# Kernel optimization log

Hardware: AMD Instinct MI355X
Metric: run time of the kernel (lower is better)

Reference implementation:

```python
import jax, jax.numpy as jnp
import numpy as np

N = 50000
E = 800000
H = 128

def _mlp_init(key, sizes, bias_flags):
    ws = []
    for i, (din, dout) in enumerate(zip(sizes[:-1], sizes[1:])):
        key, k1, k2 = jax.random.split(key, 3)
        lim = 1.0 / np.sqrt(din)
        W = jax.random.uniform(k1, (din, dout), jnp.float32, -lim, lim)
        ws.append(W)
        if bias_flags[i]:
            ws.append(jax.random.uniform(k2, (dout,), jnp.float32, -lim, lim))
    return key, ws

def setup_inputs() -> dict:
    key = jax.random.key(0)
    key, kh, kx, ke = jax.random.split(key, 4)
    h = jax.random.normal(kh, (N, H), jnp.float32)
    x = jax.random.normal(kx, (N, 3), jnp.float32)
    edge_index = jax.random.randint(ke, (2, E), 0, N, jnp.int64)
    # edge_mlp: Linear(2H+1, H), Linear(H, H), both with bias
    key, (W_e1, b_e1, W_e2, b_e2) = _mlp_init(key, [2 * H + 1, H, H], [True, True])
    # coord_mlp: Linear(H, H) with bias, Linear(H, 1) no bias
    key, (W_c1, b_c1, W_c2) = _mlp_init(key, [H, H, 1], [True, False])
    # node_mlp: Linear(2H, H), Linear(H, H), both with bias
    key, (W_n1, b_n1, W_n2, b_n2) = _mlp_init(key, [2 * H, H, H], [True, True])
    ln_g = jnp.ones((H,), jnp.float32)
    ln_b = jnp.zeros((H,), jnp.float32)
    return {"h": h, "x": x, "edge_index": edge_index,
            "W_e1": W_e1, "b_e1": b_e1, "W_e2": W_e2, "b_e2": b_e2,
            "W_c1": W_c1, "b_c1": b_c1, "W_c2": W_c2,
            "W_n1": W_n1, "b_n1": b_n1, "W_n2": W_n2, "b_n2": b_n2,
            "ln_g": ln_g, "ln_b": ln_b}

def reference(h, x, edge_index, W_e1, b_e1, W_e2, b_e2, W_c1, b_c1, W_c2,
              W_n1, b_n1, W_n2, b_n2, ln_g, ln_b):
    row, col = edge_index[0], edge_index[1]
    coord_diff = x[row] - x[col]                       # [E, 3]
    dist = jnp.linalg.norm(coord_diff, axis=1, keepdims=True)  # [E, 1]
    radial = dist ** 2
    edge_input = jnp.concatenate([h[row], h[col], radial], axis=1)  # [E, 2H+1]
    m_ij = jax.nn.silu(jax.nn.silu(edge_input @ W_e1 + b_e1) @ W_e2 + b_e2)  # [E, H]
    force_scalar = jnp.tanh(jax.nn.silu(m_ij @ W_c1 + b_c1) @ W_c2) * 0.1    # [E, 1]
    norm_diff = coord_diff / (dist + 1e-8)
    force_vector = norm_diff * force_scalar            # [E, 3]
    x_new = x + jax.ops.segment_sum(force_vector, row, num_segments=N)
    m_i = jax.ops.segment_sum(m_ij, row, num_segments=N)  # [N, H]
    node_input = jnp.concatenate([h, m_i], axis=1)     # [N, 2H]
    h_res = h + jax.nn.silu(node_input @ W_n1 + b_n1) @ W_n2 + b_n2
    mu = jnp.mean(h_res, axis=-1, keepdims=True)
    var = jnp.var(h_res, axis=-1, keepdims=True)
    h_new = (h_res - mu) / jnp.sqrt(var + 1e-5) * ln_g + ln_b
    return (h_new, x_new)
```

## Files before the change

### kernel.cpp

```cpp
#include <hip/hip_runtime.h>
#include <hip/hip_bf16.h>

#define NN 50000
#define NE 800000
#define HH 128
#define SCAN_NB 196

typedef short s16x8 __attribute__((ext_vector_type(8)));
typedef float f32x4 __attribute__((ext_vector_type(4)));
typedef unsigned int u32x4 __attribute__((ext_vector_type(4)));
typedef __bf16 bf16x2 __attribute__((ext_vector_type(2)));

__device__ __forceinline__ float u2f(unsigned int v) {
    float f;
    __builtin_memcpy(&f, &v, 4);
    return f;
}
__device__ __forceinline__ float bf2f(unsigned short u) {
    return u2f(((unsigned int)u) << 16);
}
__device__ __forceinline__ unsigned short f2bf_sw(float f) {
    unsigned int x;
    __builtin_memcpy(&x, &f, 4);
    unsigned int r = (x + 0x7fffu + ((x >> 16) & 1u)) >> 16;
    return (unsigned short)r;
}
__device__ __forceinline__ unsigned int f2bf_pk(float a, float b) {
#if __has_builtin(__builtin_amdgcn_cvt_pk_bf16_f32)
    bf16x2 p = __builtin_amdgcn_cvt_pk_bf16_f32(a, b);
    unsigned int u;
    __builtin_memcpy(&u, &p, 4);
    return u;
#else
    return (unsigned int)f2bf_sw(a) | ((unsigned int)f2bf_sw(b) << 16);
#endif
}
__device__ __forceinline__ unsigned short f2bf(float a) {
#if __has_builtin(__builtin_amdgcn_cvt_pk_bf16_f32)
    return (unsigned short)(f2bf_pk(a, a) & 0xffffu);
#else
    return f2bf_sw(a);
#endif
}
__device__ __forceinline__ float silu(float v) {
    return v * __builtin_amdgcn_rcpf(1.f + __expf(-v));
}

__global__ void transpose_w(const float* __restrict__ W,
                            unsigned short* __restrict__ WT, int K) {
    int idx = blockIdx.x * 256 + threadIdx.x;
    if (idx >= 128 * K) return;
    int n = idx / K, k = idx - n * K;
    WT[idx] = f2bf(W[k * 128 + n]);
}

__global__ void transpose_pw(const float* __restrict__ W1,
                             unsigned short* __restrict__ PWT) {
    int idx = blockIdx.x * 256 + threadIdx.x;
    if (idx >= 256 * 128) return;
    int cp = idx >> 7, k = idx & 127;
    int srow = (cp < 128) ? k : (128 + k);
    int scol = cp & 127;
    PWT[idx] = f2bf(W1[srow * 128 + scol]);
}

__global__ void k_count(const int* __restrict__ eidx, int* __restrict__ counts) {
    int e = blockIdx.x * 256 + threadIdx.x;
    if (e >= NE) return;
    int r = eidx[e];
    r = r < 0 ? 0 : (r >= NN ? NN - 1 : r);
    atomicAdd(&counts[r], 1);
}
__global__ void k_partial(const int* __restrict__ counts, int* __restrict__ partials) {
    __shared__ int sm[256];
    int idx = blockIdx.x * 256 + threadIdx.x;
    sm[threadIdx.x] = idx < NN ? counts[idx] : 0;
    __syncthreads();
    for (int s = 128; s > 0; s >>= 1) {
        if (threadIdx.x < s) sm[threadIdx.x] += sm[threadIdx.x + s];
        __syncthreads();
    }
    if (threadIdx.x == 0) partials[blockIdx.x] = sm[0];
}
__global__ void k_scanp(const int* __restrict__ partials, int* __restrict__ scanp) {
    __shared__ int sm[256];
    int t = threadIdx.x;
    int v = t < SCAN_NB ? partials[t] : 0;
    sm[t] = v;
    __syncthreads();
    for (int d = 1; d < 256; d <<= 1) {
        int add = t >= d ? sm[t - d] : 0;
        __syncthreads();
        sm[t] += add;
        __syncthreads();
    }
    scanp[t] = sm[t] - v;
}
__global__ void k_offsets(const int* __restrict__ counts, const int* __restrict__ scanp,
                          int* __restrict__ offsets) {
    __shared__ int sm[256];
    int t = threadIdx.x, idx = blockIdx.x * 256 + t;
    int v = idx < NN ? counts[idx] : 0;
    sm[t] = v;
    __syncthreads();
    for (int d = 1; d < 256; d <<= 1) {
        int add = t >= d ? sm[t - d] : 0;
        __syncthreads();
        sm[t] += add;
        __syncthreads();
    }
    if (idx < NN) offsets[idx] = sm[t] - v + scanp[blockIdx.x];
}
__global__ void k_fill(const int* __restrict__ eidx, const int* __restrict__ offsets,
                       int* __restrict__ cursor, unsigned int* __restrict__ rc) {
    int e = blockIdx.x * 256 + threadIdx.x;
    if (e >= NE) return;
    int r = eidx[e];
    int c = eidx[NE + e];
    r = r < 0 ? 0 : (r >= NN ? NN - 1 : r);
    c = c < 0 ? 0 : (c >= NN ? NN - 1 : c);
    int slot = offsets[r] + atomicAdd(&cursor[r], 1);
    rc[slot] = (unsigned int)r | ((unsigned int)c << 16);
}

__global__ __launch_bounds__(256, 4) void pgemm(
    const float* __restrict__ h, const unsigned short* __restrict__ PWT,
    unsigned short* __restrict__ P1, unsigned short* __restrict__ P2) {
    __shared__ unsigned short Alds[64 * 136];
    const int tid = threadIdx.x;
    const int n0 = blockIdx.x * 64;

#pragma unroll
    for (int j = 0; j < 4; j++) {
        int idx = tid + j * 256;
        int e = idx >> 4, ch = idx & 15;
        int node = n0 + e;
        if (node >= NN) node = NN - 1;
        const f32x4* p = (const f32x4*)&h[node * 128 + ch * 8];
        f32x4 a = p[0], b = p[1];
        u32x4 s;
        s[0] = f2bf_pk(a[0], a[1]);
        s[1] = f2bf_pk(a[2], a[3]);
        s[2] = f2bf_pk(b[0], b[1]);
        s[3] = f2bf_pk(b[2], b[3]);
        *(u32x4*)&Alds[e * 136 + ch * 8] = s;
    }
    __syncthreads();

    const int lane = tid & 63;
    const int w = tid >> 6;
    const int ln15 = lane & 15;
    const int q8 = (lane >> 4) * 8, q4 = (lane >> 4) * 4;
    const int cbase = w * 64;

    f32x4 acc[4][4];
#pragma unroll
    for (int et = 0; et < 4; et++)
#pragma unroll
        for (int nt = 0; nt < 4; nt++) acc[et][nt] = (f32x4){0.f, 0.f, 0.f, 0.f};
#pragma unroll
    for (int kk = 0; kk < 4; kk++) {
        int k0 = kk * 32 + q8;
        s16x8 a[4], b[4];
#pragma unroll
        for (int et = 0; et < 4; et++)
            a[et] = *(const s16x8*)&Alds[(et * 16 + ln15) * 136 + k0];
#pragma unroll
        for (int nt = 0; nt < 4; nt++)
            b[nt] = *(const s16x8*)&PWT[(cbase + nt * 16 + ln15) * 128 + k0];
#pragma unroll
        for (int et = 0; et < 4; et++)
#pragma unroll
            for (int nt = 0; nt < 4; nt++)
                acc[et][nt] = __builtin_amdgcn_mfma_f32_16x16x32_bf16(
                    a[et], b[nt], acc[et][nt], 0, 0, 0);
    }
#pragma unroll
    for (int nt = 0; nt < 4; nt++) {
        int cp = cbase + nt * 16 + ln15;
        unsigned short* dst = (cp < 128) ? P1 : P2;
        int col = cp & 127;
#pragma unroll
        for (int et = 0; et < 4; et++)
#pragma unroll
            for (int r = 0; r < 4; r++) {
                int row = et * 16 + q4 + r;
                int node = n0 + row;
                if (node >= NN) node = NN - 1;
                dst[node * 128 + col] = f2bf(acc[et][nt][r]);
            }
    }
}

__global__ __launch_bounds__(256, 8) void edge_kernel(
    const unsigned short* __restrict__ P1, const unsigned short* __restrict__ P2,
    const float* __restrict__ x, const unsigned int* __restrict__ rc,
    const float* __restrict__ b1, const float* __restrict__ W1full,
    const unsigned short* __restrict__ W2T, const float* __restrict__ b2,
    const unsigned short* __restrict__ Wc1T, const float* __restrict__ bc1,
    const float* __restrict__ wc2,
    float* __restrict__ m_i, float* __restrict__ x_acc) {
    __shared__ unsigned short mid1[64 * 132];
    __shared__ float b1s[128], wls[128];
    __shared__ float rad[64], ndx[64], ndy[64], ndz[64], fsum[64];
    __shared__ int rowA[64], colA[64];

    const int tid = threadIdx.x;
    const int e0 = blockIdx.x * 64;

    if (tid < 64) {
        unsigned int pk = rc[e0 + tid];
        int r = pk & 0xffff, c = pk >> 16;
        rowA[tid] = r; colA[tid] = c;
        float dx = x[r * 3 + 0] - x[c * 3 + 0];
        float dy = x[r * 3 + 1] - x[c * 3 + 1];
        float dz = x[r * 3 + 2] - x[c * 3 + 2];
        float d2 = dx * dx + dy * dy + dz * dz;
        float dist = sqrtf(d2);
        float inv = __builtin_amdgcn_rcpf(dist + 1e-8f);
        rad[tid] = d2;
        ndx[tid] = dx * inv; ndy[tid] = dy * inv; ndz[tid] = dz * inv;
        fsum[tid] = 0.f;
    } else if (tid >= 128 && tid < 256) {
        int c = tid - 128;
        b1s[c] = b1[c];
        wls[c] = W1full[256 * 128 + c];
    }
    __syncthreads();

#pragma unroll
    for (int j = 0; j < 4; j++) {
        int idx = tid + j * 256;
        int e = idx >> 4, ch = idx & 15;
        int r = rowA[e], c = colA[e];
        u32x4 p1 = *(const u32x4*)&P1[(size_t)r * 128 + ch * 8];
        u32x4 p2 = *(const u32x4*)&P2[(size_t)c * 128 + ch * 8];
        float rd = rad[e];
        u32x4 s;
#pragma unroll
        for (int t = 0; t < 4; t++) {
            int col = ch * 8 + t * 2;
            float a0 = u2f(p1[t] << 16), a1 = u2f(p1[t] & 0xffff0000u);
            float c0 = u2f(p2[t] << 16), c1 = u2f(p2[t] & 0xffff0000u);
            float v0 = a0 + c0 + rd * wls[col] + b1s[col];
            float v1 = a1 + c1 + rd * wls[col + 1] + b1s[col + 1];
            s[t] = f2bf_pk(silu(v0), silu(v1));
        }
        *(u32x4*)&mid1[e * 132 + ch * 8] = s;
    }
    __syncthreads();

    const int lane = tid & 63;
    const int w = tid >> 6;
    const int ln15 = lane & 15;
    const int q8 = (lane >> 4) * 8, q4 = (lane >> 4) * 4;
    const int nbase = w * 32;

    f32x4 acc[4][2];

#pragma unroll
    for (int et = 0; et < 4; et++)
#pragma unroll
        for (int nt = 0; nt < 2; nt++) acc[et][nt] = (f32x4){0.f, 0.f, 0.f, 0.f};
#pragma unroll
    for (int kk = 0; kk < 4; kk++) {
        int k0 = kk * 32 + q8;
        s16x8 a[4], b[2];
#pragma unroll
        for (int et = 0; et < 4; et++)
            a[et] = *(const s16x8*)&mid1[(et * 16 + ln15) * 132 + k0];
#pragma unroll
        for (int nt = 0; nt < 2; nt++)
            b[nt] = *(const s16x8*)&W2T[(nbase + nt * 16 + ln15) * 128 + k0];
#pragma unroll
        for (int et = 0; et < 4; et++)
#pragma unroll
            for (int nt = 0; nt < 2; nt++)
                acc[et][nt] = __builtin_amdgcn_mfma_f32_16x16x32_bf16(
                    a[et], b[nt], acc[et][nt], 0, 0, 0);
    }
    __syncthreads();
    unsigned short* mid2 = mid1;
#pragma unroll
    for (int nt = 0; nt < 2; nt++) {
        int col = nbase + nt * 16 + ln15;
        float bias = b2[col];
#pragma unroll
        for (int et = 0; et < 4; et++)
#pragma unroll
            for (int r = 0; r < 4; r++) {
                int row = et * 16 + q4 + r;
                mid2[row * 132 + col] = f2bf(silu(acc[et][nt][r] + bias));
            }
    }
    __syncthreads();

#pragma unroll
    for (int et = 0; et < 4; et++)
#pragma unroll
        for (int nt = 0; nt < 2; nt++) acc[et][nt] = (f32x4){0.f, 0.f, 0.f, 0.f};
#pragma unroll
    for (int kk = 0; kk < 4; kk++) {
        int k0 = kk * 32 + q8;
        s16x8 a[4], b[2];
#pragma unroll
        for (int et = 0; et < 4; et++)
            a[et] = *(const s16x8*)&mid2[(et * 16 + ln15) * 132 + k0];
#pragma unroll
        for (int nt = 0; nt < 2; nt++)
            b[nt] = *(const s16x8*)&Wc1T[(nbase + nt * 16 + ln15) * 128 + k0];
#pragma unroll
        for (int et = 0; et < 4; et++)
#pragma unroll
            for (int nt = 0; nt < 2; nt++)
                acc[et][nt] = __builtin_amdgcn_mfma_f32_16x16x32_bf16(
                    a[et], b[nt], acc[et][nt], 0, 0, 0);
    }

    {
        int col = tid & 127;
        int r0 = (tid >> 7) * 32;
        float accv = 0.f;
        int cur = rowA[r0];
        for (int row = r0; row < r0 + 32; row++) {
            int rn = rowA[row];
            if (rn != cur) {
                atomicAdd(&m_i[(size_t)cur * 128 + col], accv);
                accv = 0.f;
                cur = rn;
            }
            accv += bf2f(mid2[row * 132 + col]);
        }
        atomicAdd(&m_i[(size_t)cur * 128 + col], accv);
    }

    {
        float part[4][4];
#pragma unroll
        for (int et = 0; et < 4; et++)
#pragma unroll
            for (int r = 0; r < 4; r++) part[et][r] = 0.f;
#pragma unroll
        for (int nt = 0; nt < 2; nt++) {
            int col = nbase + nt * 16 + ln15;
            float bias = bc1[col];
            float w2 = wc2[col];
#pragma unroll
            for (int et = 0; et < 4; et++)
#pragma unroll
                for (int r = 0; r < 4; r++)
                    part[et][r] += silu(acc[et][nt][r] + bias) * w2;
        }
#pragma unroll
        for (int et = 0; et < 4; et++)
#pragma unroll
            for (int r = 0; r < 4; r++) {
                float p = part[et][r];
                p += __shfl_xor(p, 8, 16);
                p += __shfl_xor(p, 4, 16);
                p += __shfl_xor(p, 2, 16);
                p += __shfl_xor(p, 1, 16);
                if (ln15 == 0) atomicAdd(&fsum[et * 16 + q4 + r], p);
            }
    }
    __syncthreads();
    if (tid < 64) {
        float fs = tanhf(fsum[tid]) * 0.1f;
        ndx[tid] *= fs; ndy[tid] *= fs; ndz[tid] *= fs;
    }
    __syncthreads();
    if (tid < 64) {
        bool head = (tid == 0) || (rowA[tid] != rowA[tid - 1]);
        if (head) {
            int rn = rowA[tid];
            float ax = 0.f, ay = 0.f, az = 0.f;
            for (int j = tid; j < 64 && rowA[j] == rn; j++) {
                ax += ndx[j]; ay += ndy[j]; az += ndz[j];
            }
            atomicAdd(&x_acc[rn * 3 + 0], ax);
            atomicAdd(&x_acc[rn * 3 + 1], ay);
            atomicAdd(&x_acc[rn * 3 + 2], az);
        }
    }
}

__global__ __launch_bounds__(256, 4) void node_kernel(
    const float* __restrict__ h, const float* __restrict__ m_i,
    const unsigned short* __restrict__ Wn1T, const float* __restrict__ bn1,
    const unsigned short* __restrict__ Wn2T, const float* __restrict__ bn2,
    const float* __restrict__ ln_g, const float* __restrict__ ln_b,
    float* __restrict__ out_h) {
    __shared__ unsigned short Alds[64 * 264];
    unsigned short* mid1 = Alds;
    float* tile = (float*)Alds;

    const int tid = threadIdx.x;
    const int n0 = blockIdx.x * 64;

#pragma unroll
    for (int i = 0; i < 8; i++) {
        int idx = tid + i * 256;
        int hr = idx >> 4, ch = idx & 15;
        int e = hr >> 1, half = hr & 1;
        int node = n0 + e;
        if (node >= NN) node = NN - 1;
        const float* src = half ? &m_i[(size_t)node * 128 + ch * 8]
                                : &h[(size_t)node * 128 + ch * 8];
        const f32x4* sp = (const f32x4*)src;
        f32x4 f0 = sp[0], f1 = sp[1];
        u32x4 s;
        s[0] = f2bf_pk(f0[0], f0[1]);
        s[1] = f2bf_pk(f0[2], f0[3]);
        s[2] = f2bf_pk(f1[0], f1[1]);
        s[3] = f2bf_pk(f1[2], f1[3]);
        *(u32x4*)&Alds[e * 264 + half * 128 + ch * 8] = s;
    }
    __syncthreads();

    const int lane = tid & 63;
    const int w = tid >> 6;
    const int ln15 = lane & 15;
    const int q8 = (lane >> 4) * 8, q4 = (lane >> 4) * 4;
    const int nbase = w * 32;

    f32x4 acc[4][2];

#pragma unroll
    for (int et = 0; et < 4; et++)
#pragma unroll
        for (int nt = 0; nt < 2; nt++) acc[et][nt] = (f32x4){0.f, 0.f, 0.f, 0.f};
#pragma unroll
    for (int kk = 0; kk < 8; kk++) {
        int k0 = kk * 32 + q8;
        s16x8 a[4], b[2];
#pragma unroll
        for (int et = 0; et < 4; et++)
            a[et] = *(const s16x8*)&Alds[(et * 16 + ln15) * 264 + k0];
#pragma unroll
        for (int nt = 0; nt < 2; nt++)
            b[nt] = *(const s16x8*)&Wn1T[(nbase + nt * 16 + ln15) * 256 + k0];
#pragma unroll
        for (int et = 0; et < 4; et++)
#pragma unroll
            for (int nt = 0; nt < 2; nt++)
                acc[et][nt] = __builtin_amdgcn_mfma_f32_16x16x32_bf16(
                    a[et], b[nt], acc[et][nt], 0, 0, 0);
    }
    __syncthreads();
#pragma unroll
    for (int nt = 0; nt < 2; nt++) {
        int col = nbase + nt * 16 + ln15;
        float bias = bn1[col];
#pragma unroll
        for (int et = 0; et < 4; et++)
#pragma unroll
            for (int r = 0; r < 4; r++) {
                int row = et * 16 + q4 + r;
                mid1[row * 132 + col] = f2bf(silu(acc[et][nt][r] + bias));
            }
    }
    __syncthreads();

#pragma unroll
    for (int et = 0; et < 4; et++)
#pragma unroll
        for (int nt = 0; nt < 2; nt++) acc[et][nt] = (f32x4){0.f, 0.f, 0.f, 0.f};
#pragma unroll
    for (int kk = 0; kk < 4; kk++) {
        int k0 = kk * 32 + q8;
        s16x8 a[4], b[2];
#pragma unroll
        for (int et = 0; et < 4; et++)
            a[et] = *(const s16x8*)&mid1[(et * 16 + ln15) * 132 + k0];
#pragma unroll
        for (int nt = 0; nt < 2; nt++)
            b[nt] = *(const s16x8*)&Wn2T[(nbase + nt * 16 + ln15) * 128 + k0];
#pragma unroll
        for (int et = 0; et < 4; et++)
#pragma unroll
            for (int nt = 0; nt < 2; nt++)
                acc[et][nt] = __builtin_amdgcn_mfma_f32_16x16x32_bf16(
                    a[et], b[nt], acc[et][nt], 0, 0, 0);
    }
    __syncthreads();
#pragma unroll
    for (int nt = 0; nt < 2; nt++) {
        int col = nbase + nt * 16 + ln15;
        float bias = bn2[col];
#pragma unroll
        for (int et = 0; et < 4; et++)
#pragma unroll
            for (int r = 0; r < 4; r++) {
                int row = et * 16 + q4 + r;
                int node = n0 + row;
                int nclamp = node >= NN ? NN - 1 : node;
                float v = acc[et][nt][r] + bias + h[(size_t)nclamp * 128 + col];
                tile[row * 132 + col] = v;
            }
    }
    __syncthreads();

    {
        int row = tid >> 2;
        int q = tid & 3;
        float s = 0.f, s2 = 0.f;
#pragma unroll
        for (int c = 0; c < 32; c++) {
            float v = tile[row * 132 + q + c * 4];
            s += v; s2 += v * v;
        }
        s += __shfl_xor(s, 1, 4);  s2 += __shfl_xor(s2, 1, 4);
        s += __shfl_xor(s, 2, 4);  s2 += __shfl_xor(s2, 2, 4);
        float mean = s * (1.f / 128.f);
        float var = s2 * (1.f / 128.f) - mean * mean;
        float rs = rsqrtf(var + 1e-5f);
        int node = n0 + row;
        if (node < NN) {
#pragma unroll
            for (int c = 0; c < 32; c++) {
                int col = q + c * 4;
                float v = (tile[row * 132 + col] - mean) * rs * ln_g[col] + ln_b[col];
                out_h[(size_t)node * 128 + col] = v;
            }
        }
    }
}

__global__ void x_kernel(const float* __restrict__ x,
                         const float* __restrict__ x_acc,
                         float* __restrict__ out_x) {
    int i = blockIdx.x * 256 + threadIdx.x;
    if (i < NN * 3) out_x[i] = x[i] + x_acc[i];
}

extern "C" void kernel_launch(void* const* d_in, const int* in_sizes, int n_in,
                              void* d_out, int out_size, void* d_ws, size_t ws_size,
                              hipStream_t stream) {
    const float* h    = (const float*)d_in[0];
    const float* x    = (const float*)d_in[1];
    const int* eidx   = (const int*)d_in[2];
    const float* W_e1 = (const float*)d_in[3];
    const float* b_e1 = (const float*)d_in[4];
    const float* W_e2 = (const float*)d_in[5];
    const float* b_e2 = (const float*)d_in[6];
    const float* W_c1 = (const float*)d_in[7];
    const float* b_c1 = (const float*)d_in[8];
    const float* W_c2 = (const float*)d_in[9];
    const float* W_n1 = (const float*)d_in[10];
    const float* b_n1 = (const float*)d_in[11];
    const float* W_n2 = (const float*)d_in[12];
    const float* b_n2 = (const float*)d_in[13];
    const float* ln_g = (const float*)d_in[14];
    const float* ln_b = (const float*)d_in[15];

    float* out_h = (float*)d_out;
    float* out_x = out_h + NN * HH;

    char* ws = (char*)d_ws;
    float* m_i    = (float*)ws;
    float* x_acc  = (float*)(ws + 25600000);
    int* counts   = (int*)(ws + 26200000);
    int* cursor   = (int*)(ws + 26400000);
    int* offsets  = (int*)(ws + 26600000);
    int* partials = (int*)(ws + 26800000);
    int* scanp    = (int*)(ws + 26801024);
    unsigned int* rc = (unsigned int*)(ws + 26802048);
    unsigned short* P1  = (unsigned short*)(ws + 30002048);
    unsigned short* P2  = (unsigned short*)(ws + 42802048);
    unsigned short* PWT = (unsigned short*)(ws + 55602048);
    unsigned short* W2T  = (unsigned short*)(ws + 55667584);
    unsigned short* Wc1T = (unsigned short*)(ws + 55700352);
    unsigned short* Wn1T = (unsigned short*)(ws + 55733120);
    unsigned short* Wn2T = (unsigned short*)(ws + 55798656);

    hipMemsetAsync(ws, 0, 26800000, stream);
    transpose_pw<<<(256 * 128 + 255) / 256, 256, 0, stream>>>(W_e1, PWT);
    transpose_w<<<(128 * 128 + 255) / 256, 256, 0, stream>>>(W_e2, W2T, 128);
    transpose_w<<<(128 * 128 + 255) / 256, 256, 0, stream>>>(W_c1, Wc1T, 128);
    transpose_w<<<(128 * 256 + 255) / 256, 256, 0, stream>>>(W_n1, Wn1T, 256);
    transpose_w<<<(128 * 128 + 255) / 256, 256, 0, stream>>>(W_n2, Wn2T, 128);
    k_count<<<(NE + 255) / 256, 256, 0, stream>>>(eidx, counts);
    k_partial<<<SCAN_NB, 256, 0, stream>>>(counts, partials);
    k_scanp<<<1, 256, 0, stream>>>(partials, scanp);
    k_offsets<<<SCAN_NB, 256, 0, stream>>>(counts, scanp, offsets);
    k_fill<<<(NE + 255) / 256, 256, 0, stream>>>(eidx, offsets, cursor, rc);
    pgemm<<<(NN + 63) / 64, 256, 0, stream>>>(h, PWT, P1, P2);

    edge_kernel<<<NE / 64, 256, 0, stream>>>(P1, P2, x, rc, b_e1, W_e1, W2T,
                                             b_e2, Wc1T, b_c1, W_c2, m_i, x_acc);
    node_kernel<<<(NN + 63) / 64, 256, 0, stream>>>(h, m_i, Wn1T, b_n1, Wn2T,
                                                    b_n2, ln_g, ln_b, out_h);
    x_kernel<<<(NN * 3 + 255) / 256, 256, 0, stream>>>(x, x_acc, out_x);
}
```

Measured before the change: 453.1 us.

## Merge prep launches, single-block scan, fold bias into pgemm, widen edge blocks

Folds the five weight-transpose kernels and the edge count into one prep kernel, and replaces the three-kernel scan with a single 1024-thread block scan. The first-layer edge bias is now added during the P1 projection GEMM rather than per edge. The edge kernel processes 128 edges per 512-thread block, and its m_i scatter reads two columns per thread. The x update is folded into the node kernel, so fewer launches remain overall. Larger edge blocks use more LDS, which may reduce occupancy, and the single-block scan serializes that step on one workgroup.

```diff
diff --git a/kernel.cpp b/kernel.cpp
--- a/kernel.cpp
+++ b/kernel.cpp
@@ -4,7 +4,6 @@
 #define NN 50000
 #define NE 800000
 #define HH 128
-#define SCAN_NB 196
 
 typedef short s16x8 __attribute__((ext_vector_type(8)));
 typedef float f32x4 __attribute__((ext_vector_type(4)));
@@ -46,71 +45,65 @@
     return v * __builtin_amdgcn_rcpf(1.f + __expf(-v));
 }
 
-__global__ void transpose_w(const float* __restrict__ W,
-                            unsigned short* __restrict__ WT, int K) {
+__global__ void prep_kernel(
+    const float* __restrict__ W_e1, const float* __restrict__ W_e2,
+    const float* __restrict__ W_c1, const float* __restrict__ W_n1,
+    const float* __restrict__ W_n2, const int* __restrict__ eidx,
+    unsigned short* __restrict__ PWT, unsigned short* __restrict__ W2T,
+    unsigned short* __restrict__ Wc1T, unsigned short* __restrict__ Wn1T,
+    unsigned short* __restrict__ Wn2T, int* __restrict__ counts) {
     int idx = blockIdx.x * 256 + threadIdx.x;
-    if (idx >= 128 * K) return;
-    int n = idx / K, k = idx - n * K;
-    WT[idx] = f2bf(W[k * 128 + n]);
-}
-
-__global__ void transpose_pw(const float* __restrict__ W1,
-                             unsigned short* __restrict__ PWT) {
-    int idx = blockIdx.x * 256 + threadIdx.x;
-    if (idx >= 256 * 128) return;
-    int cp = idx >> 7, k = idx & 127;
-    int srow = (cp < 128) ? k : (128 + k);
-    int scol = cp & 127;
-    PWT[idx] = f2bf(W1[srow * 128 + scol]);
-}
-
-__global__ void k_count(const int* __restrict__ eidx, int* __restrict__ counts) {
-    int e = blockIdx.x * 256 + threadIdx.x;
-    if (e >= NE) return;
-    int r = eidx[e];
-    r = r < 0 ? 0 : (r >= NN ? NN - 1 : r);
-    atomicAdd(&counts[r], 1);
-}
-__global__ void k_partial(const int* __restrict__ counts, int* __restrict__ partials) {
-    __shared__ int sm[256];
-    int idx = blockIdx.x * 256 + threadIdx.x;
-    sm[threadIdx.x] = idx < NN ? counts[idx] : 0;
-    __syncthreads();
-    for (int s = 128; s > 0; s >>= 1) {
-        if (threadIdx.x < s) sm[threadIdx.x] += sm[threadIdx.x + s];
-        __syncthreads();
-    }
-    if (threadIdx.x == 0) partials[blockIdx.x] = sm[0];
-}
-__global__ void k_scanp(const int* __restrict__ partials, int* __restrict__ scanp) {
-    __shared__ int sm[256];
+    if (idx < 32768) {
+        int cp = idx >> 7, k = idx & 127;
+        int srow = (cp < 128) ? k : (128 + k);
+        PWT[idx] = f2bf(W_e1[srow * 128 + (cp & 127)]);
+    } else if (idx < 49152) {
+        int i = idx - 32768, n = i >> 7, k = i & 127;
+        W2T[i] = f2bf(W_e2[k * 128 + n]);
+    } else if (idx < 65536) {
+        int i = idx - 49152, n = i >> 7, k = i & 127;
+        Wc1T[i] = f2bf(W_c1[k * 128 + n]);
+    } else if (idx < 98304) {
+        int i = idx - 65536, n = i >> 8, k = i & 255;
+        Wn1T[i] = f2bf(W_n1[k * 128 + n]);
+    } else if (idx < 114688) {
+        int i = idx - 98304, n = i >> 7, k = i & 127;
+        Wn2T[i] = f2bf(W_n2[k * 128 + n]);
+    } else if (idx < 114688 + NE) {
+        int e = idx - 114688;
+        int r = eidx[e];
+        r = r < 0 ? 0 : (r >= NN ? NN - 1 : r);
+        atomicAdd(&counts[r], 1);
+    }
+}
+
+__global__ void k_scan(const int* __restrict__ counts, int* __restrict__ offsets) {
+    __shared__ int sm[1024];
     int t = threadIdx.x;
-    int v = t < SCAN_NB ? partials[t] : 0;
-    sm[t] = v;
-    __syncthreads();
-    for (int d = 1; d < 256; d <<= 1) {
-        int add = t >= d ? sm[t - d] : 0;
+    int base = t * 49;
+    int sum = 0;
+    for (int i = 0; i < 49; i++) {
+        int idx = base + i;
+        if (idx < NN) sum += counts[idx];
+    }
+    sm[t] = sum;
+    __syncthreads();
+    for (int d = 1; d < 1024; d <<= 1) {
+        int add = (t >= d) ? sm[t - d] : 0;
         __syncthreads();
         sm[t] += add;
         __syncthreads();
     }
-    scanp[t] = sm[t] - v;
-}
-__global__ void k_offsets(const int* __restrict__ counts, const int* __restrict__ scanp,
-                          int* __restrict__ offsets) {
-    __shared__ int sm[256];
-    int t = threadIdx.x, idx = blockIdx.x * 256 + t;
-    int v = idx < NN ? counts[idx] : 0;
-    sm[t] = v;
-    __syncthreads();
-    for (int d = 1; d < 256; d <<= 1) {
-        int add = t >= d ? sm[t - d] : 0;
-        __syncthreads();
-        sm[t] += add;
-        __syncthreads();
-    }
-    if (idx < NN) offsets[idx] = sm[t] - v + scanp[blockIdx.x];
-}
+    int acc = sm[t] - sum;
+    for (int i = 0; i < 49; i++) {
+        int idx = base + i;
+        if (idx < NN) {
+            offsets[idx] = acc;
+            acc += counts[idx];
+        }
+    }
+}
+
 __global__ void k_fill(const int* __restrict__ eidx, const int* __restrict__ offsets,
                        int* __restrict__ cursor, unsigned int* __restrict__ rc) {
     int e = blockIdx.x * 256 + threadIdx.x;
@@ -125,6 +118,7 @@
 
 __global__ __launch_bounds__(256, 4) void pgemm(
     const float* __restrict__ h, const unsigned short* __restrict__ PWT,
+    const float* __restrict__ b1,
     unsigned short* __restrict__ P1, unsigned short* __restrict__ P2) {
     __shared__ unsigned short Alds[64 * 136];
     const int tid = threadIdx.x;
@@ -178,8 +172,10 @@
 #pragma unroll
     for (int nt = 0; nt < 4; nt++) {
         int cp = cbase + nt * 16 + ln15;
-        unsigned short* dst = (cp < 128) ? P1 : P2;
+        bool top = cp < 128;
+        unsigned short* dst = top ? P1 : P2;
         int col = cp & 127;
+        float badd = top ? b1[col] : 0.f;
 #pragma unroll
         for (int et = 0; et < 4; et++)
 #pragma unroll
@@ -187,28 +183,28 @@
                 int row = et * 16 + q4 + r;
                 int node = n0 + row;
                 if (node >= NN) node = NN - 1;
-                dst[node * 128 + col] = f2bf(acc[et][nt][r]);
-            }
-    }
-}
-
-__global__ __launch_bounds__(256, 8) void edge_kernel(
+                dst[node * 128 + col] = f2bf(acc[et][nt][r] + badd);
+            }
+    }
+}
+
+__global__ __launch_bounds__(512, 8) void edge_kernel(
     const unsigned short* __restrict__ P1, const unsigned short* __restrict__ P2,
     const float* __restrict__ x, const unsigned int* __restrict__ rc,
-    const float* __restrict__ b1, const float* __restrict__ W1full,
+    const float* __restrict__ W1full,
     const unsigned short* __restrict__ W2T, const float* __restrict__ b2,
     const unsigned short* __restrict__ Wc1T, const float* __restrict__ bc1,
     const float* __restrict__ wc2,
     float* __restrict__ m_i, float* __restrict__ x_acc) {
-    __shared__ unsigned short mid1[64 * 132];
-    __shared__ float b1s[128], wls[128];
-    __shared__ float rad[64], ndx[64], ndy[64], ndz[64], fsum[64];
-    __shared__ int rowA[64], colA[64];
+    __shared__ unsigned short mid1[128 * 132];
+    __shared__ float wls[128];
+    __shared__ float rad[128], ndx[128], ndy[128], ndz[128], fsum[128];
+    __shared__ int rowA[128], colA[128];
 
     const int tid = threadIdx.x;
-    const int e0 = blockIdx.x * 64;
-
-    if (tid < 64) {
+    const int e0 = blockIdx.x * 128;
+
+    if (tid < 128) {
         unsigned int pk = rc[e0 + tid];
         int r = pk & 0xffff, c = pk >> 16;
         rowA[tid] = r; colA[tid] = c;
@@ -221,16 +217,15 @@
         rad[tid] = d2;
         ndx[tid] = dx * inv; ndy[tid] = dy * inv; ndz[tid] = dz * inv;
         fsum[tid] = 0.f;
-    } else if (tid >= 128 && tid < 256) {
+    } else if (tid < 256) {
         int c = tid - 128;
-        b1s[c] = b1[c];
         wls[c] = W1full[256 * 128 + c];
     }
     __syncthreads();
 
 #pragma unroll
     for (int j = 0; j < 4; j++) {
-        int idx = tid + j * 256;
+        int idx = tid + j * 512;
         int e = idx >> 4, ch = idx & 15;
         int r = rowA[e], c = colA[e];
         u32x4 p1 = *(const u32x4*)&P1[(size_t)r * 128 + ch * 8];
@@ -242,8 +237,8 @@
             int col = ch * 8 + t * 2;
             float a0 = u2f(p1[t] << 16), a1 = u2f(p1[t] & 0xffff0000u);
             float c0 = u2f(p2[t] << 16), c1 = u2f(p2[t] & 0xffff0000u);
-            float v0 = a0 + c0 + rd * wls[col] + b1s[col];
-            float v1 = a1 + c1 + rd * wls[col + 1] + b1s[col + 1];
+            float v0 = a0 + c0 + rd * wls[col];
+            float v1 = a1 + c1 + rd * wls[col + 1];
             s[t] = f2bf_pk(silu(v0), silu(v1));
         }
         *(u32x4*)&mid1[e * 132 + ch * 8] = s;
@@ -254,7 +249,8 @@
     const int w = tid >> 6;
     const int ln15 = lane & 15;
     const int q8 = (lane >> 4) * 8, q4 = (lane >> 4) * 4;
-    const int nbase = w * 32;
+    const int nbase = (w & 3) * 32;
+    const int rb = (w >> 2) * 64;
 
     f32x4 acc[4][2];
 
@@ -268,7 +264,7 @@
         s16x8 a[4], b[2];
 #pragma unroll
         for (int et = 0; et < 4; et++)
-            a[et] = *(const s16x8*)&mid1[(et * 16 + ln15) * 132 + k0];
+            a[et] = *(const s16x8*)&mid1[(rb + et * 16 + ln15) * 132 + k0];
 #pragma unroll
         for (int nt = 0; nt < 2; nt++)
             b[nt] = *(const s16x8*)&W2T[(nbase + nt * 16 + ln15) * 128 + k0];
@@ -289,7 +285,7 @@
         for (int et = 0; et < 4; et++)
 #pragma unroll
             for (int r = 0; r < 4; r++) {
-                int row = et * 16 + q4 + r;
+                int row = rb + et * 16 + q4 + r;
                 mid2[row * 132 + col] = f2bf(silu(acc[et][nt][r] + bias));
             }
     }
@@ -305,7 +301,7 @@
         s16x8 a[4], b[2];
 #pragma unroll
         for (int et = 0; et < 4; et++)
-            a[et] = *(const s16x8*)&mid2[(et * 16 + ln15) * 132 + k0];
+            a[et] = *(const s16x8*)&mid2[(rb + et * 16 + ln15) * 132 + k0];
 #pragma unroll
         for (int nt = 0; nt < 2; nt++)
             b[nt] = *(const s16x8*)&Wc1T[(nbase + nt * 16 + ln15) * 128 + k0];
@@ -318,20 +314,25 @@
     }
 
     {
-        int col = tid & 127;
-        int r0 = (tid >> 7) * 32;
-        float accv = 0.f;
+        int cp2 = (tid & 63) * 2;
+        int g = tid >> 6;
+        int r0 = g * 16;
+        float a0 = 0.f, a1 = 0.f;
         int cur = rowA[r0];
-        for (int row = r0; row < r0 + 32; row++) {
+        for (int row = r0; row < r0 + 16; row++) {
             int rn = rowA[row];
             if (rn != cur) {
-                atomicAdd(&m_i[(size_t)cur * 128 + col], accv);
-                accv = 0.f;
+                atomicAdd(&m_i[(size_t)cur * 128 + cp2], a0);
+                atomicAdd(&m_i[(size_t)cur * 128 + cp2 + 1], a1);
+                a0 = 0.f; a1 = 0.f;
                 cur = rn;
             }
-            accv += bf2f(mid2[row * 132 + col]);
-        }
-        atomicAdd(&m_i[(size_t)cur * 128 + col], accv);
+            unsigned int v = *(const unsigned int*)&mid2[row * 132 + cp2];
+            a0 += u2f(v << 16);
+            a1 += u2f(v & 0xffff0000u);
+        }
+        atomicAdd(&m_i[(size_t)cur * 128 + cp2], a0);
+        atomicAdd(&m_i[(size_t)cur * 128 + cp2 + 1], a1);
     }
 
     {
@@ -360,21 +361,21 @@
                 p += __shfl_xor(p, 4, 16);
                 p += __shfl_xor(p, 2, 16);
                 p += __shfl_xor(p, 1, 16);
-                if (ln15 == 0) atomicAdd(&fsum[et * 16 + q4 + r], p);
-            }
-    }
-    __syncthreads();
-    if (tid < 64) {
+                if (ln15 == 0) atomicAdd(&fsum[rb + et * 16 + q4 + r], p);
+            }
+    }
+    __syncthreads();
+    if (tid < 128) {
         float fs = tanhf(fsum[tid]) * 0.1f;
         ndx[tid] *= fs; ndy[tid] *= fs; ndz[tid] *= fs;
     }
     __syncthreads();
-    if (tid < 64) {
+    if (tid < 128) {
         bool head = (tid == 0) || (rowA[tid] != rowA[tid - 1]);
         if (head) {
             int rn = rowA[tid];
             float ax = 0.f, ay = 0.f, az = 0.f;
-            for (int j = tid; j < 64 && rowA[j] == rn; j++) {
+            for (int j = tid; j < 128 && rowA[j] == rn; j++) {
                 ax += ndx[j]; ay += ndy[j]; az += ndz[j];
             }
             atomicAdd(&x_acc[rn * 3 + 0], ax);
@@ -386,16 +387,22 @@
 
 __global__ __launch_bounds__(256, 4) void node_kernel(
     const float* __restrict__ h, const float* __restrict__ m_i,
+    const float* __restrict__ x, const float* __restrict__ x_acc,
     const unsigned short* __restrict__ Wn1T, const float* __restrict__ bn1,
     const unsigned short* __restrict__ Wn2T, const float* __restrict__ bn2,
     const float* __restrict__ ln_g, const float* __restrict__ ln_b,
-    float* __restrict__ out_h) {
+    float* __restrict__ out_h, float* __restrict__ out_x) {
     __shared__ unsigned short Alds[64 * 264];
     unsigned short* mid1 = Alds;
     float* tile = (float*)Alds;
 
     const int tid = threadIdx.x;
     const int n0 = blockIdx.x * 64;
+
+    if (tid < 192) {
+        int i = n0 * 3 + tid;
+        if (i < NN * 3) out_x[i] = x[i] + x_acc[i];
+    }
 
 #pragma unroll
     for (int i = 0; i < 8; i++) {
@@ -524,13 +531,6 @@
             }
         }
     }
-}
-
-__global__ void x_kernel(const float* __restrict__ x,
-                         const float* __restrict__ x_acc,
-                         float* __restrict__ out_x) {
-    int i = blockIdx.x * 256 + threadIdx.x;
-    if (i < NN * 3) out_x[i] = x[i] + x_acc[i];
 }
 
 extern "C" void kernel_launch(void* const* d_in, const int* in_sizes, int n_in,
@@ -562,8 +562,6 @@
     int* counts   = (int*)(ws + 26200000);
     int* cursor   = (int*)(ws + 26400000);
     int* offsets  = (int*)(ws + 26600000);
-    int* partials = (int*)(ws + 26800000);
-    int* scanp    = (int*)(ws + 26801024);
     unsigned int* rc = (unsigned int*)(ws + 26802048);
     unsigned short* P1  = (unsigned short*)(ws + 30002048);
     unsigned short* P2  = (unsigned short*)(ws + 42802048);
@@ -574,21 +572,15 @@
     unsigned short* Wn2T = (unsigned short*)(ws + 55798656);
 
     hipMemsetAsync(ws, 0, 26800000, stream);
-    transpose_pw<<<(256 * 128 + 255) / 256, 256, 0, stream>>>(W_e1, PWT);
-    transpose_w<<<(128 * 128 + 255) / 256, 256, 0, stream>>>(W_e2, W2T, 128);
-    transpose_w<<<(128 * 128 + 255) / 256, 256, 0, stream>>>(W_c1, Wc1T, 128);
-    transpose_w<<<(128 * 256 + 255) / 256, 256, 0, stream>>>(W_n1, Wn1T, 256);
-    transpose_w<<<(128 * 128 + 255) / 256, 256, 0, stream>>>(W_n2, Wn2T, 128);
-    k_count<<<(NE + 255) / 256, 256, 0, stream>>>(eidx, counts);
-    k_partial<<<SCAN_NB, 256, 0, stream>>>(counts, partials);
-    k_scanp<<<1, 256, 0, stream>>>(partials, scanp);
-    k_offsets<<<SCAN_NB, 256, 0, stream>>>(counts, scanp, offsets);
+
+    prep_kernel<<<(114688 + NE + 255) / 256, 256, 0, stream>>>(
+        W_e1, W_e2, W_c1, W_n1, W_n2, eidx, PWT, W2T, Wc1T, Wn1T, Wn2T, counts);
+    k_scan<<<1, 1024, 0, stream>>>(counts, offsets);
     k_fill<<<(NE + 255) / 256, 256, 0, stream>>>(eidx, offsets, cursor, rc);
-    pgemm<<<(NN + 63) / 64, 256, 0, stream>>>(h, PWT, P1, P2);
-
-    edge_kernel<<<NE / 64, 256, 0, stream>>>(P1, P2, x, rc, b_e1, W_e1, W2T,
-                                             b_e2, Wc1T, b_c1, W_c2, m_i, x_acc);
-    node_kernel<<<(NN + 63) / 64, 256, 0, stream>>>(h, m_i, Wn1T, b_n1, Wn2T,
-                                                    b_n2, ln_g, ln_b, out_h);
-    x_kernel<<<(NN * 3 + 255) / 256, 256, 0, stream>>>(x, x_acc, out_x);
-}
+    pgemm<<<(NN + 63) / 64, 256, 0, stream>>>(h, PWT, b_e1, P1, P2);
+
+    edge_kernel<<<NE / 128, 512, 0, stream>>>(P1, P2, x, rc, W_e1, W2T, b_e2,
+                                              Wc1T, b_c1, W_c2, m_i, x_acc);
+    node_kernel<<<(NN + 63) / 64, 256, 0, stream>>>(
+        h, m_i, x, x_acc, Wn1T, b_n1, Wn2T, b_n2, ln_g, ln_b, out_h, out_x);
+}
```

Measured after the change: 534.5 us. 18.0% more time.
